# Optimization experiments

Hardware: AMD Instinct MI355X
Metric: run time of the kernel (lower is better)

The kernel has to match this reference:

```python
import jax, jax.numpy as jnp
import numpy as np

# Mex config (matches init_kwargs)
B, C, H, W = 64, 64, 64, 64
BLK = (64, 3, 3)        # block over (C, H, W); spans all channels -> out_c = 1
STR = (64, 2, 2)
PAD = (0, 1, 1)
NI = 256                # num_instances
EPS = 1.0
SOFTMAX_MODE = False    # False -> mean (logsumexp - log k), True -> plain logsumexp


def setup_inputs() -> dict:
    key = jax.random.key(0)
    k1, k2 = jax.random.split(key)
    x = jax.random.normal(k1, (B, C, H, W), dtype=jnp.float32)
    kblk = BLK[0] * BLK[1] * BLK[2]
    # Dirichlet([1]*k) init == normalized exponentials; nregions = 1 (shared offsets)
    e = jax.random.exponential(k2, (1, NI, kblk), dtype=jnp.float32)
    offsets = (e / jnp.sum(e, axis=-1, keepdims=True)).reshape(1, NI, *BLK)
    return {"x": x, "offsets": offsets}


def _mex_forward(x, offsets):
    eps = jnp.float32(EPS)
    bc, bh, bw = BLK
    # im2col patch extraction: (B, C*bh*bw, OH, OW); feature dim ordered (c, fh, fw)
    patches = jax.lax.conv_general_dilated_patches(
        x, (bh, bw), (STR[1], STR[2]),
        [(PAD[1], PAD[1]), (PAD[2], PAD[2])],  # zero padding == blocks_out_of_bounds_value
        dimension_numbers=("NCHW", "OIHW", "NCHW"),
    )
    Bn, K, OH, OW = patches.shape  # K = bc*bh*bw = 576
    P = patches.transpose(0, 2, 3, 1).reshape(-1, K)  # (N, k), N = B*OH*OW
    O = offsets.reshape(NI, K)                         # single shared region

    # y_ni = (1/eps) * logsumexp_k( eps*(P_nk + O_ik) ) - log(k)/eps (mean mode)
    # exp-domain GEMM with max-shift for stability:
    Pe = eps * P
    Oe = eps * O
    mp = jnp.max(Pe, axis=1, keepdims=True)   # (N, 1)
    mo = jnp.max(Oe, axis=1, keepdims=True)   # (I, 1)
    S = jnp.exp(Pe - mp) @ jnp.exp(Oe - mo).T  # (N, I)
    y = (jnp.log(S) + mp + mo.T) / eps
    if not SOFTMAX_MODE:
        y = y - jnp.log(jnp.float32(K)) / eps
    # output: (B, num_instances * out_c, OH, OW) with out_c = 1
    return y.reshape(Bn, OH, OW, NI).transpose(0, 3, 1, 2)


def reference(x, offsets):
    return _mex_forward(x, offsets)
```

## Files before the change

kernel.cpp:

```cpp
#include <hip/hip_runtime.h>
#include <hip/hip_bf16.h>


typedef __bf16 bf16x8 __attribute__((ext_vector_type(8)));
typedef float  f32x4  __attribute__((ext_vector_type(4)));

__global__ void mex_prep_b(const float* __restrict__ off, __bf16* __restrict__ Bt) {
    const int i = blockIdx.x * 4 + (threadIdx.x >> 6);
    const int c = threadIdx.x & 63;
    const int c8 = c >> 3, j = c & 7;
    const int wv = i >> 6, nt = (i >> 4) & 3, t16 = i & 15;
    const int q  = c8 & 3;
    const float* oi = off + i * 576;
    #pragma unroll
    for (int p = 0; p < 9; ++p) {
        float v = oi[c * 9 + p];
        const int ks    = p * 2 + (c8 >> 2);
        const int chunk = (ks * 16 + wv * 4 + nt) * 64 + q * 16 + t16;
        Bt[chunk * 8 + j] = (__bf16)__expf(v);
    }
}

__global__ __launch_bounds__(256, 2) void mex_main(
        const float* __restrict__ x,
        const __bf16* __restrict__ Bt,
        float* __restrict__ out) {
    __shared__ bf16x8 lds8[2 * 2560];

    const int bid = blockIdx.x;
    const int wid  = ((bid & 7) << 6) | (bid >> 3);
    const int b    = wid >> 3;
    const int j2   = wid & 7;
    const int oh0a = j2 << 2;
    const int oh0b = oh0a + 2;
    const int tid  = threadIdx.x;
    const int wv   = tid >> 6;
    const int lane = tid & 63;

    bf16x8 one8;
    #pragma unroll
    for (int j = 0; j < 8; ++j) one8[j] = (__bf16)1.0f;

    if (oh0a == 0) {
        #pragma unroll
        for (int i = 0; i < 2; ++i) lds8[tid + i * 256] = one8;
    }

    const int wp  = tid & 31;
    const int w0  = wp << 1;
    const int c8  = tid >> 5;
    const int c8p = c8 ^ (wp & 7);
    const float* xb = x + ((size_t)b << 18) + w0;

    #pragma unroll
    for (int hl = 0; hl < 5; ++hl) {
        const int hg = 2 * oh0a - 1 + hl;
        if (hg >= 0) {
            const float* xp = xb + (hg << 6);
            float2 v[8];
            #pragma unroll
            for (int k = 0; k < 8; ++k)
                v[k] = *(const float2*)(xp + (((c8 << 3) + k) << 12));
            bf16x8 ca, cb;
            #pragma unroll
            for (int k = 0; k < 8; ++k) {
                ca[k] = (__bf16)__expf(v[k].x);
                cb[k] = (__bf16)__expf(v[k].y);
            }
            bf16x8* dst = lds8 + hl * 512 + w0 * 8 + c8p;
            dst[0] = ca;
            dst[8] = cb;
        }
    }

    float2 v1[40];
    const float* xc = xb + (((oh0b << 1) - 1) << 6) + ((size_t)c8 << 15);

    const bf16x8* __restrict__ Btv = (const bf16x8*)Bt;
    const int wv4 = wv << 2;
    bf16x8 b0[4], b1[4];
    #pragma unroll
    for (int nt = 0; nt < 4; ++nt) {
        b0[nt] = Btv[(wv4 + nt) * 64 + lane];
        b1[nt] = Btv[(16 + wv4 + nt) * 64 + lane];
    }

    const int t16 = tid & 15;
    const int q   = (tid >> 4) & 3;
    int hb[4], wo2[4];
    #pragma unroll
    for (int mt = 0; mt < 4; ++mt) {
        const int m = mt * 16 + t16;
        wo2[mt] = (m & 31) << 1;
        hb[mt]  = (m >> 5) << 7;
    }
    const float lK = 6.356107660695891f;

    f32x4 acc0[4][4], acc1[4][4];
    #pragma unroll
    for (int mt = 0; mt < 4; ++mt)
        #pragma unroll
        for (int nt = 0; nt < 4; ++nt) acc0[mt][nt] = (f32x4)(0.0f);

    __syncthreads();

    #pragma unroll
    for (int ks = 0; ks < 18; ++ks) {
        const int p  = ks >> 1;
        const int fh = (p * 11) >> 5;
        const int fw = p - fh * 3;
        const int ccq = ((ks & 1) << 2) + q;
        bf16x8 a[4];
        #pragma unroll
        for (int mt = 0; mt < 4; ++mt) {
            const int wc  = wo2[mt] + fw - 1;
            const int pad = wc < 0;
            const int wcl = pad ? 0 : wc;
            const int row = hb[mt] + fh * 64 + wcl;
            bf16x8 vv = lds8[row * 8 + (ccq ^ ((wcl >> 1) & 7))];
            a[mt] = pad ? one8 : vv;
        }
        bf16x8 b2[4];
        if (ks < 16) {
            #pragma unroll
            for (int nt = 0; nt < 4; ++nt)
                b2[nt] = Btv[((ks + 2) * 16 + wv4 + nt) * 64 + lane];
        }
        if (ks < 16) {
            #pragma unroll
            for (int u = 0; u < 2; ++u) {
                const int k = 2 * ks + u;
                v1[k] = *(const float2*)(xc + (k >> 3) * 64 + ((k & 7) << 12));
            }
        } else {
            #pragma unroll
            for (int u = 0; u < 4; ++u) {
                const int k = 32 + ((ks - 16) << 2) + u;
                v1[k] = *(const float2*)(xc + (k >> 3) * 64 + ((k & 7) << 12));
            }
        }
        #pragma unroll
        for (int mt = 0; mt < 4; ++mt)
            #pragma unroll
            for (int nt = 0; nt < 4; ++nt)
                acc0[mt][nt] = __builtin_amdgcn_mfma_f32_16x16x32_bf16(
                    a[mt], b0[nt], acc0[mt][nt], 0, 0, 0);
        #pragma unroll
        for (int nt = 0; nt < 4; ++nt) { b0[nt] = b1[nt]; b1[nt] = b2[nt]; }
    }

    #pragma unroll
    for (int hl = 0; hl < 5; ++hl) {
        bf16x8 ca, cb;
        #pragma unroll
        for (int k = 0; k < 8; ++k) {
            ca[k] = (__bf16)__expf(v1[hl * 8 + k].x);
            cb[k] = (__bf16)__expf(v1[hl * 8 + k].y);
        }
        bf16x8* dst = lds8 + 2560 + hl * 512 + w0 * 8 + c8p;
        dst[0] = ca;
        dst[8] = cb;
    }
    #pragma unroll
    for (int nt = 0; nt < 4; ++nt) {
        b0[nt] = Btv[(wv4 + nt) * 64 + lane];
        b1[nt] = Btv[(16 + wv4 + nt) * 64 + lane];
    }
    #pragma unroll
    for (int mt = 0; mt < 4; ++mt)
        #pragma unroll
        for (int nt = 0; nt < 4; ++nt) acc1[mt][nt] = (f32x4)(0.0f);

    __syncthreads();

    #pragma unroll
    for (int ks = 0; ks < 18; ++ks) {
        const int p  = ks >> 1;
        const int fh = (p * 11) >> 5;
        const int fw = p - fh * 3;
        const int ccq = ((ks & 1) << 2) + q;
        bf16x8 a[4];
        #pragma unroll
        for (int mt = 0; mt < 4; ++mt) {
            const int wc  = wo2[mt] + fw - 1;
            const int pad = wc < 0;
            const int wcl = pad ? 0 : wc;
            const int row = hb[mt] + fh * 64 + wcl;
            bf16x8 vv = lds8[2560 + row * 8 + (ccq ^ ((wcl >> 1) & 7))];
            a[mt] = pad ? one8 : vv;
        }
        bf16x8 b2[4];
        if (ks < 16) {
            #pragma unroll
            for (int nt = 0; nt < 4; ++nt)
                b2[nt] = Btv[((ks + 2) * 16 + wv4 + nt) * 64 + lane];
        }
        if (ks < 16) {
            const int emt = ks >> 2, ent = ks & 3;
            const int m    = emt * 16 + (q << 2);
            const int ohl  = m >> 5;
            const int owi  = m & 31;
            const int orow = (oh0a + ohl) * 32 + owi;
            const int inst = wv * 64 + ent * 16 + t16;
            f32x4 r;
            #pragma unroll
            for (int j = 0; j < 4; ++j)
                r[j] = __logf(acc0[emt][ent][j]) - lK;
            *(f32x4*)(out + (((size_t)b * 256 + inst) * 1024 + orow)) = r;
        }
        #pragma unroll
        for (int mt = 0; mt < 4; ++mt)
            #pragma unroll
            for (int nt = 0; nt < 4; ++nt)
                acc1[mt][nt] = __builtin_amdgcn_mfma_f32_16x16x32_bf16(
                    a[mt], b0[nt], acc1[mt][nt], 0, 0, 0);
        #pragma unroll
        for (int nt = 0; nt < 4; ++nt) { b0[nt] = b1[nt]; b1[nt] = b2[nt]; }
    }

    #pragma unroll
    for (int mt = 0; mt < 4; ++mt) {
        const int m   = mt * 16 + (q << 2);
        const int ohl = m >> 5;
        const int owi = m & 31;
        const int orow = (oh0b + ohl) * 32 + owi;
        #pragma unroll
        for (int nt = 0; nt < 4; ++nt) {
            const int inst = wv * 64 + nt * 16 + t16;
            f32x4 r;
            #pragma unroll
            for (int j = 0; j < 4; ++j)
                r[j] = __logf(acc1[mt][nt][j]) - lK;
            *(f32x4*)(out + (((size_t)b * 256 + inst) * 1024 + orow)) = r;
        }
    }
}

extern "C" void kernel_launch(void* const* d_in, const int* in_sizes, int n_in,
                              void* d_out, int out_size, void* d_ws, size_t ws_size,
                              hipStream_t stream) {
    const float* x   = (const float*)d_in[0];
    const float* off = (const float*)d_in[1];
    float* out = (float*)d_out;
    __bf16* Bt = (__bf16*)d_ws;

    mex_prep_b<<<64, 256, 0, stream>>>(off, Bt);
    mex_main<<<512, 256, 0, stream>>>(x, Bt, out);
}
```

Measured before the change: 130.5 us.

## Reuse shared halo row and overlap second-tile exp/LDS stores with first GEMM

```diff
diff --git a/kernel.cpp b/kernel.cpp
--- a/kernel.cpp
+++ b/kernel.cpp
@@ -73,8 +73,8 @@
         }
     }
 
-    float2 v1[40];
-    const float* xc = xb + (((oh0b << 1) - 1) << 6) + ((size_t)c8 << 15);
+    float2 v1[4][8];
+    const float* xc2 = xb + (((oh0a << 1) + 4) << 6) + ((size_t)c8 << 15);
 
     const bf16x8* __restrict__ Btv = (const bf16x8*)Bt;
     const int wv4 = wv << 2;
@@ -126,18 +126,24 @@
             for (int nt = 0; nt < 4; ++nt)
                 b2[nt] = Btv[((ks + 2) * 16 + wv4 + nt) * 64 + lane];
         }
-        if (ks < 16) {
-            #pragma unroll
-            for (int u = 0; u < 2; ++u) {
-                const int k = 2 * ks + u;
-                v1[k] = *(const float2*)(xc + (k >> 3) * 64 + ((k & 7) << 12));
+        if (ks < 8) {
+            const int r = ks >> 1, u0 = (ks & 1) << 2;
+            #pragma unroll
+            for (int u = 0; u < 4; ++u)
+                v1[r][u0 + u] =
+                    *(const float2*)(xc2 + r * 64 + ((u0 + u) << 12));
+        }
+        if (ks >= 4 && ks <= 10 && (ks & 1) == 0) {
+            const int r = (ks - 4) >> 1;
+            bf16x8 ca, cb;
+            #pragma unroll
+            for (int k = 0; k < 8; ++k) {
+                ca[k] = (__bf16)__expf(v1[r][k].x);
+                cb[k] = (__bf16)__expf(v1[r][k].y);
             }
-        } else {
-            #pragma unroll
-            for (int u = 0; u < 4; ++u) {
-                const int k = 32 + ((ks - 16) << 2) + u;
-                v1[k] = *(const float2*)(xc + (k >> 3) * 64 + ((k & 7) << 12));
-            }
+            bf16x8* dst = lds8 + 2560 + (r + 1) * 512 + w0 * 8 + c8p;
+            dst[0] = ca;
+            dst[8] = cb;
         }
         #pragma unroll
         for (int mt = 0; mt < 4; ++mt)
@@ -149,18 +155,6 @@
         for (int nt = 0; nt < 4; ++nt) { b0[nt] = b1[nt]; b1[nt] = b2[nt]; }
     }
 
-    #pragma unroll
-    for (int hl = 0; hl < 5; ++hl) {
-        bf16x8 ca, cb;
-        #pragma unroll
-        for (int k = 0; k < 8; ++k) {
-            ca[k] = (__bf16)__expf(v1[hl * 8 + k].x);
-            cb[k] = (__bf16)__expf(v1[hl * 8 + k].y);
-        }
-        bf16x8* dst = lds8 + 2560 + hl * 512 + w0 * 8 + c8p;
-        dst[0] = ca;
-        dst[8] = cb;
-    }
     #pragma unroll
     for (int nt = 0; nt < 4; ++nt) {
         b0[nt] = Btv[(wv4 + nt) * 64 + lane];
@@ -185,8 +179,10 @@
             const int wc  = wo2[mt] + fw - 1;
             const int pad = wc < 0;
             const int wcl = pad ? 0 : wc;
-            const int row = hb[mt] + fh * 64 + wcl;
-            bf16x8 vv = lds8[2560 + row * 8 + (ccq ^ ((wcl >> 1) & 7))];
+            const bf16x8* bse = (mt < 2 && fh == 0)
+                ? (lds8 + 4 * 512)
+                : (lds8 + 2560 + (hb[mt] + fh * 64) * 8);
+            bf16x8 vv = bse[wcl * 8 + (ccq ^ ((wcl >> 1) & 7))];
             a[mt] = pad ? one8 : vv;
         }
         bf16x8 b2[4];
```

New measurement: 138.8 us. 1.06x slower.
